# Kernel tuning notes

Measured on AMD Instinct MI355X. Metric: run time of the kernel, lower is better.

The kernel has to match this reference:

```python
import jax, jax.numpy as jnp
import numpy as np

T, B, DIM, N, K = 512, 32, 1024, 256, 32  # K = checkpoint interval, divides T


def setup_inputs() -> dict:
    key = jax.random.key(0)
    k1, k2, k3, k4 = jax.random.split(key, 4)
    scale = 1.0 / np.sqrt(DIM)  # keep projections O(1) like trained weights
    return {
        "x": jax.random.normal(k1, (T, B, DIM), dtype=jnp.float32),
        "S0": jnp.zeros((B, N, N), dtype=jnp.float32),
        "W_k": jax.random.normal(k2, (N, DIM), dtype=jnp.float32) * scale,
        "W_v": jax.random.normal(k3, (N, DIM), dtype=jnp.float32) * scale,
        "W_q": jax.random.normal(k4, (N, DIM), dtype=jnp.float32) * scale,
    }


def reference(x, S0, W_k, W_v, W_q):
    # Projections (batched GEMMs), done once up-front as in the torch code.
    k_all = jnp.einsum("tbd,nd->tbn", x, W_k)
    v_all = jnp.einsum("tbd,nd->tbn", x, W_v)
    q_all = jnp.einsum("tbd,nd->tbn", x, W_q)
    k_norm = k_all / (jnp.linalg.norm(k_all, axis=-1, keepdims=True) + 1e-6)

    def step(S, kvq):
        kn, v, q = kvq  # each [B, N]
        retrieved = jnp.einsum("bij,bj->bi", S, kn)          # S @ k_norm
        S = S + (v - retrieved)[:, :, None] * kn[:, None, :]  # rank-1 delta write
        Sq = jnp.einsum("bij,bj->bi", S, q)                   # readout with updated S
        out = Sq * jax.nn.silu(Sq)
        return S, out

    def segment(S, kvq_seg):
        return jax.lax.scan(step, S, kvq_seg)

    nseg = T // K
    seg_kvq = (
        k_norm.reshape(nseg, K, B, N),
        v_all.reshape(nseg, K, B, N),
        q_all.reshape(nseg, K, B, N),
    )
    _, outs = jax.lax.scan(segment, S0, seg_kvq)  # [nseg, K, B, N]
    return outs.reshape(T, B, N)
```

## Files before the change

kernel.cpp:

```cpp
#include <hip/hip_runtime.h>
#include <hip/hip_bf16.h>
#include <math.h>

#define T_DIM 512
#define B_DIM 32
#define D_DIM 1024
#define N_DIM 256
#define M_DIM (T_DIM * B_DIM)
#define CHUNK 32
#define NCHUNK (T_DIM / CHUNK)
#define IBLK 32
#define ST (B_DIM * N_DIM)
#define BK 32

typedef _Float16 f16;
typedef _Float16 f16x8 __attribute__((ext_vector_type(8)));
typedef _Float16 f16x4 __attribute__((ext_vector_type(4)));
typedef _Float16 f16x2 __attribute__((ext_vector_type(2)));
typedef __fp16   h16x2 __attribute__((ext_vector_type(2)));
typedef float    f32x4 __attribute__((ext_vector_type(4)));

#define LDK 264
#define LDT 40
#define LDV 36

#define GLOAD_LDS16(g, l)                                         \
  __builtin_amdgcn_global_load_lds(                               \
      (const __attribute__((address_space(1))) void*)(g),         \
      (__attribute__((address_space(3))) void*)(l), 16, 0, 0)

__device__ __forceinline__ f16x8 cvt8(const float4& a, const float4& b) {
  f16x8 h;
  h[0] = (f16)a.x; h[1] = (f16)a.y; h[2] = (f16)a.z; h[3] = (f16)a.w;
  h[4] = (f16)b.x; h[5] = (f16)b.y; h[6] = (f16)b.z; h[7] = (f16)b.w;
  return h;
}

__device__ __forceinline__ f16x8 pk8(const f32x4 a, const f32x4 b) {
  union { f16x8 v; h16x2 p[4]; } u;
  u.p[0] = __builtin_amdgcn_cvt_pkrtz(a[0], a[1]);
  u.p[1] = __builtin_amdgcn_cvt_pkrtz(a[2], a[3]);
  u.p[2] = __builtin_amdgcn_cvt_pkrtz(b[0], b[1]);
  u.p[3] = __builtin_amdgcn_cvt_pkrtz(b[2], b[3]);
  return u.v;
}

__global__ __launch_bounds__(256) void cvt_w_kernel(
    const float* __restrict__ wk, const float* __restrict__ wv,
    const float* __restrict__ wq, f16* __restrict__ out) {
  const int i = (blockIdx.x * 256 + threadIdx.x) * 8;
  const int m = blockIdx.y;
  const float* src = (m == 0) ? wk : (m == 1) ? wv : wq;
  const float4 f0 = *(const float4*)(src + i);
  const float4 f1 = *(const float4*)(src + i + 4);
  *(f16x8*)(out + (size_t)m * (N_DIM * D_DIM) + i) = cvt8(f0, f1);
}

__global__ __launch_bounds__(256, 3) void proj_gemm_mfma(
    const float* __restrict__ x, const f16* __restrict__ Wh,
    f16* __restrict__ ok, f16* __restrict__ ov, f16* __restrict__ oq) {
  __shared__ __align__(16) float Af[2][128 * BK];
  __shared__ __align__(16) f16   Bh[2][128 * BK];

  const int tid  = threadIdx.x;
  const int lane = tid & 63;
  const int w    = tid >> 6;
  const int wm   = w >> 1, wn = w & 1;
  const int lr   = lane & 15;
  const int lq   = lane >> 4;

  const int mb  = blockIdx.x * 128;
  const int mat = blockIdx.y >> 1;
  const int nb  = (blockIdx.y & 1) * 128;

  const f16* Wmat = Wh + (size_t)mat * (N_DIM * D_DIM) + (size_t)nb * D_DIM;
  f16*       C    = (mat == 0) ? ok : (mat == 1) ? ov : oq;

  const int ar  = lane >> 3;
  const int acq = (lane & 7) ^ ar;
  const int brr = lane >> 2;
  const int bco = lane & 3;

  f32x4 acc[4][4];
  #pragma unroll
  for (int i = 0; i < 4; ++i)
    #pragma unroll
    for (int j = 0; j < 4; ++j) acc[i][j] = (f32x4){0.f, 0.f, 0.f, 0.f};

  #pragma unroll
  for (int j = 0; j < 4; ++j) {
    const int r = 32 * j + 8 * w + ar;
    GLOAD_LDS16(x + (size_t)(mb + r) * D_DIM + acq * 4, &Af[0][(32 * j + 8 * w) * BK]);
  }
  #pragma unroll
  for (int j = 0; j < 2; ++j) {
    const int r = 64 * j + 16 * w + brr;
    GLOAD_LDS16(Wmat + (size_t)r * D_DIM + bco * 8, &Bh[0][(64 * j + 16 * w) * BK]);
  }
  __syncthreads();

  int cur = 0;
  for (int kt = 0; kt < D_DIM; kt += BK) {
    if (kt + BK < D_DIM) {
      #pragma unroll
      for (int j = 0; j < 4; ++j) {
        const int r = 32 * j + 8 * w + ar;
        GLOAD_LDS16(x + (size_t)(mb + r) * D_DIM + kt + BK + acq * 4,
                    &Af[cur ^ 1][(32 * j + 8 * w) * BK]);
      }
      #pragma unroll
      for (int j = 0; j < 2; ++j) {
        const int r = 64 * j + 16 * w + brr;
        GLOAD_LDS16(Wmat + (size_t)r * D_DIM + kt + BK + bco * 8,
                    &Bh[cur ^ 1][(64 * j + 16 * w) * BK]);
      }
    }
    {
      f16x8 af[4], bf[4];
      #pragma unroll
      for (int mi = 0; mi < 4; ++mi) {
        const int row = 64 * wm + 16 * mi + lr;
        const int q0  = (2 * lq)     ^ (row & 7);
        const int q1  = (2 * lq + 1) ^ (row & 7);
        const f32x4 a0 = *(const f32x4*)&Af[cur][row * BK + q0 * 4];
        const f32x4 a1 = *(const f32x4*)&Af[cur][row * BK + q1 * 4];
        af[mi] = pk8(a0, a1);
      }
      #pragma unroll
      for (int nj = 0; nj < 4; ++nj) {
        const int row = 64 * wn + 16 * nj + lr;
        bf[nj] = *(const f16x8*)&Bh[cur][row * BK + lq * 8];
      }
      #pragma unroll
      for (int mi = 0; mi < 4; ++mi)
        #pragma unroll
        for (int nj = 0; nj < 4; ++nj)
          acc[mi][nj] = __builtin_amdgcn_mfma_f32_16x16x32_f16(af[mi], bf[nj], acc[mi][nj], 0, 0, 0);
    }
    __syncthreads();
    cur ^= 1;
  }

  #pragma unroll
  for (int mi = 0; mi < 4; ++mi)
    #pragma unroll
    for (int nj = 0; nj < 4; ++nj)
      #pragma unroll
      for (int r = 0; r < 4; ++r) {
        const int rg = mb + 64 * wm + 16 * mi + 4 * lq + r;
        const int cg = nb + 64 * wn + 16 * nj + lr;
        C[(size_t)rg * N_DIM + cg] = (f16)acc[mi][nj][r];
      }
}

__global__ __launch_bounds__(256) void knorm_kernel(f16* __restrict__ k) {
  const int w    = threadIdx.x >> 6;
  const int lane = threadIdx.x & 63;
  const int row  = blockIdx.x * 4 + w;
  f16* p = k + (size_t)row * N_DIM + lane * 4;
  f16x4 h = *reinterpret_cast<const f16x4*>(p);
  const float x0 = (float)h[0], x1 = (float)h[1], x2 = (float)h[2], x3 = (float)h[3];
  float ss = x0 * x0 + x1 * x1 + x2 * x2 + x3 * x3;
  #pragma unroll
  for (int m = 1; m < 64; m <<= 1) ss += __shfl_xor(ss, m, 64);
  const float inv = 1.0f / (sqrtf(ss) + 1e-6f);
  h[0] = (f16)(x0 * inv); h[1] = (f16)(x1 * inv);
  h[2] = (f16)(x2 * inv); h[3] = (f16)(x3 * inv);
  *reinterpret_cast<f16x4*>(p) = h;
}

__global__ __launch_bounds__(256, 2) void precompute_wg(
    const f16* __restrict__ kn, const f16* __restrict__ q,
    f16* __restrict__ Wg, f16* __restrict__ Gg, f16* __restrict__ KTg) {
  __shared__ __align__(16) f16 Kh[32 * LDK];
  __shared__ __align__(16) f16 Qh[32 * LDK];
  __shared__ float Al[32 * 33];

  const int tid  = threadIdx.x;
  const int lane = tid & 63;
  const int w    = tid >> 6;
  const int lr   = lane & 15;
  const int lq   = lane >> 4;
  const int tm   = w >> 1, tn = w & 1;
  const int b    = blockIdx.x >> 4;
  const int c    = blockIdx.x & 15;
  const int t0g  = c * CHUNK;

  {
    const int t = tid >> 3, cg = tid & 7;
    const f16* ks = kn + (size_t)(t0g + t) * ST + b * N_DIM + cg * 32;
    const f16* qs = q  + (size_t)(t0g + t) * ST + b * N_DIM + cg * 32;
    #pragma unroll
    for (int m = 0; m < 4; ++m) {
      *(f16x8*)&Kh[t * LDK + cg * 32 + 8 * m] = ((const f16x8*)ks)[m];
      *(f16x8*)&Qh[t * LDK + cg * 32 + 8 * m] = ((const f16x8*)qs)[m];
    }
  }
  __syncthreads();

  {
    f16* kt_dst = KTg + ((size_t)blockIdx.x * N_DIM + tid) * CHUNK;
    #pragma unroll
    for (int t8 = 0; t8 < 4; ++t8) {
      f16x8 h;
      #pragma unroll
      for (int e = 0; e < 8; ++e) h[e] = Kh[(8 * t8 + e) * LDK + tid];
      *(f16x8*)(kt_dst + 8 * t8) = h;
    }
  }

  f32x4 Aa = {0.f, 0.f, 0.f, 0.f}, Ga = {0.f, 0.f, 0.f, 0.f};
  #pragma unroll
  for (int kk = 0; kk < 8; ++kk) {
    f16x8 ka = *(const f16x8*)&Kh[(16 * tm + lr) * LDK + 32 * kk + 8 * lq];
    f16x8 qa = *(const f16x8*)&Qh[(16 * tm + lr) * LDK + 32 * kk + 8 * lq];
    f16x8 kb = *(const f16x8*)&Kh[(16 * tn + lr) * LDK + 32 * kk + 8 * lq];
    Aa = __builtin_amdgcn_mfma_f32_16x16x32_f16(ka, kb, Aa, 0, 0, 0);
    Ga = __builtin_amdgcn_mfma_f32_16x16x32_f16(qa, kb, Ga, 0, 0, 0);
  }
  {
    const int s = 16 * tn + lr;
    f16* gdst = Gg + (size_t)blockIdx.x * 1280;
    #pragma unroll
    for (int r = 0; r < 4; ++r) {
      const int t = 16 * tm + 4 * lq + r;
      Al[t * 33 + s] = (s < t) ? Aa[r] : 0.f;
      gdst[t * LDT + s] = (f16)((s <= t) ? Ga[r] : 0.f);
    }
  }
  __syncthreads();

  if (tid < 32) {
    float wv[32];
    f16* wdst = Wg + (size_t)blockIdx.x * 1280;
    #pragma unroll
    for (int t = 0; t < 32; ++t) {
      float s0 = 0.f, s1 = 0.f, s2 = 0.f, s3 = 0.f;
      #pragma unroll
      for (int s = 0; s < 32; ++s) {
        if (s >= t) break;
        const float a = Al[t * 33 + s];
        if ((s & 3) == 0) s0 = fmaf(a, wv[s], s0);
        else if ((s & 3) == 1) s1 = fmaf(a, wv[s], s1);
        else if ((s & 3) == 2) s2 = fmaf(a, wv[s], s2);
        else s3 = fmaf(a, wv[s], s3);
      }
      wv[t] = ((t == tid) ? 1.f : 0.f) - ((s0 + s1) + (s2 + s3));
    }
    #pragma unroll
    for (int t = 0; t < 32; ++t) wdst[t * LDT + tid] = (f16)wv[t];
  }
}

__global__ __launch_bounds__(512, 1) void scan_chunked(
    const f16* __restrict__ kn, const f16* __restrict__ v,
    const f16* __restrict__ q, const float* __restrict__ S0,
    const f16* __restrict__ Wg, const f16* __restrict__ Gg,
    const f16* __restrict__ KTg, float* __restrict__ out) {
  __shared__ __align__(16) f16 Kh[32 * LDK];
  __shared__ __align__(16) f16 Qh[32 * LDK];
  __shared__ __align__(16) f16 Sh[32 * LDK];
  __shared__ __align__(16) f16 KhT[256 * LDT];
  __shared__ __align__(16) f16 Wl[32 * LDT];
  __shared__ __align__(16) f16 Gl[32 * LDT];
  __shared__ __align__(16) f16 U0T[32 * LDT];
  __shared__ __align__(16) f16 UT[32 * LDT];
  __shared__ __align__(16) float Vl[32 * LDV];

  const int tid  = threadIdx.x;
  const int lane = tid & 63;
  const int w    = tid >> 6;
  const int lr   = lane & 15;
  const int lq   = lane >> 4;
  const int role = w >> 2;
  const int w4   = w & 3;
  const int tm   = w4 >> 1, tn = w4 & 1;
  const int b    = blockIdx.x & 31;
  const int i0   = (blockIdx.x >> 5) * IBLK;

  f32x4 acc[2][2];
  const float* S0b = S0 + (size_t)b * N_DIM * N_DIM + (size_t)i0 * N_DIM;
  #pragma unroll
  for (int ti = 0; ti < 2; ++ti)
    #pragma unroll
    for (int jt = 0; jt < 2; ++jt)
      #pragma unroll
      for (int r = 0; r < 4; ++r) {
        const int i = 16 * ti + 4 * lq + r;
        const int j = 32 * w + 16 * jt + lr;
        acc[ti][jt][r] = S0b[(size_t)i * N_DIM + j];
      }
  {
    const int i = tid >> 4, cg = tid & 15;
    const float* ss = S0b + (size_t)i * N_DIM + cg * 16;
    #pragma unroll
    for (int m = 0; m < 2; ++m) {
      float4 f0 = *(const float4*)(ss + 8 * m);
      float4 f1 = *(const float4*)(ss + 8 * m + 4);
      *(f16x8*)&Sh[i * LDK + cg * 16 + 8 * m] = cvt8(f0, f1);
    }
  }
  __syncthreads();

  for (int c = 0; c < NCHUNK; ++c) {
    const int t0g = c * CHUNK;
    {
      const int t = tid >> 4, cg = tid & 15;
      const f16* ks = kn + (size_t)(t0g + t) * ST + b * N_DIM + cg * 16;
      const f16* qs = q  + (size_t)(t0g + t) * ST + b * N_DIM + cg * 16;
      #pragma unroll
      for (int m = 0; m < 2; ++m) {
        *(f16x8*)&Kh[t * LDK + cg * 16 + 8 * m] = ((const f16x8*)ks)[m];
        *(f16x8*)&Qh[t * LDK + cg * 16 + 8 * m] = ((const f16x8*)qs)[m];
      }
      const int c2 = (tid & 15) * 2;
      const f16x2 vf = *(const f16x2*)(v + (size_t)(t0g + t) * ST + b * N_DIM + i0 + c2);
      *(float2*)&Vl[t * LDV + c2] = make_float2((float)vf[0], (float)vf[1]);
    }
    {
      const int row = tid >> 1, m0 = (tid & 1) * 2;
      const f16* src = KTg + ((size_t)(b * NCHUNK + c) * N_DIM + row) * CHUNK;
      #pragma unroll
      for (int m = 0; m < 2; ++m)
        *(f16x8*)&KhT[row * LDT + 8 * (m0 + m)] = ((const f16x8*)src)[m0 + m];
    }
    if (tid < 160) {
      ((f16x8*)Wl)[tid] = ((const f16x8*)(Wg + (size_t)(b * NCHUNK + c) * 1280))[tid];
    } else if (tid < 320) {
      ((f16x8*)Gl)[tid - 160] = ((const f16x8*)(Gg + (size_t)(b * NCHUNK + c) * 1280))[tid - 160];
    }
    __syncthreads();

    f32x4 Oq = {0.f, 0.f, 0.f, 0.f};
    if (role == 0) {
      f32x4 Pacc = {0.f, 0.f, 0.f, 0.f};
      #pragma unroll
      for (int kk = 0; kk < 8; ++kk) {
        f16x8 ka = *(const f16x8*)&Kh[(16 * tm + lr) * LDK + 32 * kk + 8 * lq];
        f16x8 sb = *(const f16x8*)&Sh[(16 * tn + lr) * LDK + 32 * kk + 8 * lq];
        Pacc = __builtin_amdgcn_mfma_f32_16x16x32_f16(ka, sb, Pacc, 0, 0, 0);
      }
      const int i = 16 * tn + lr;
      const int t0 = 16 * tm + 4 * lq;
      f16x4 u0;
      #pragma unroll
      for (int r = 0; r < 4; ++r) u0[r] = (f16)(Vl[(t0 + r) * LDV + i] - Pacc[r]);
      *(f16x4*)&U0T[i * LDT + t0] = u0;
    } else {
      #pragma unroll
      for (int kk = 0; kk < 8; ++kk) {
        f16x8 qa = *(const f16x8*)&Qh[(16 * tm + lr) * LDK + 32 * kk + 8 * lq];
        f16x8 sb = *(const f16x8*)&Sh[(16 * tn + lr) * LDK + 32 * kk + 8 * lq];
        Oq = __builtin_amdgcn_mfma_f32_16x16x32_f16(qa, sb, Oq, 0, 0, 0);
      }
    }
    __syncthreads();

    if (role == 0) {
      f16x8 wa = *(const f16x8*)&Wl[(16 * tm + lr) * LDT + 8 * lq];
      f16x8 ub = *(const f16x8*)&U0T[(16 * tn + lr) * LDT + 8 * lq];
      f32x4 z = {0.f, 0.f, 0.f, 0.f};
      f32x4 Ud = __builtin_amdgcn_mfma_f32_16x16x32_f16(wa, ub, z, 0, 0, 0);
      const int i = 16 * tn + lr;
      const int t0 = 16 * tm + 4 * lq;
      f16x4 uh;
      #pragma unroll
      for (int r = 0; r < 4; ++r) uh[r] = (f16)Ud[r];
      *(f16x4*)&UT[i * LDT + t0] = uh;
    }
    __syncthreads();

    if (role == 1) {
      f16x8 ga = *(const f16x8*)&Gl[(16 * tm + lr) * LDT + 8 * lq];
      f16x8 ub = *(const f16x8*)&UT[(16 * tn + lr) * LDT + 8 * lq];
      f32x4 O = __builtin_amdgcn_mfma_f32_16x16x32_f16(ga, ub, Oq, 0, 0, 0);
      const int i = 16 * tn + lr;
      const int tt0 = 16 * tm + 4 * lq;
      #pragma unroll
      for (int r = 0; r < 4; ++r) {
        const float sq = O[r];
        const float sig = 1.0f / (1.0f + __expf(-sq));
        out[(size_t)(t0g + tt0 + r) * ST + b * N_DIM + i0 + i] = sq * sq * sig;
      }
    }
    #pragma unroll
    for (int ti = 0; ti < 2; ++ti) {
      f16x8 ua = *(const f16x8*)&UT[(16 * ti + lr) * LDT + 8 * lq];
      #pragma unroll
      for (int jt = 0; jt < 2; ++jt) {
        f16x8 kb = *(const f16x8*)&KhT[(32 * w + 16 * jt + lr) * LDT + 8 * lq];
        acc[ti][jt] = __builtin_amdgcn_mfma_f32_16x16x32_f16(ua, kb, acc[ti][jt], 0, 0, 0);
      }
    }
    #pragma unroll
    for (int ti = 0; ti < 2; ++ti)
      #pragma unroll
      for (int jt = 0; jt < 2; ++jt)
        #pragma unroll
        for (int r = 0; r < 4; ++r)
          Sh[(16 * ti + 4 * lq + r) * LDK + 32 * w + 16 * jt + lr] = (f16)acc[ti][jt][r];
    __syncthreads();
  }
}

extern "C" void kernel_launch(void* const* d_in, const int* in_sizes, int n_in,
                              void* d_out, int out_size, void* d_ws, size_t ws_size,
                              hipStream_t stream) {
  (void)in_sizes; (void)n_in; (void)out_size; (void)ws_size;
  const float* x  = (const float*)d_in[0];
  const float* S0 = (const float*)d_in[1];
  const float* Wk = (const float*)d_in[2];
  const float* Wv = (const float*)d_in[3];
  const float* Wq = (const float*)d_in[4];
  float* outp = (float*)d_out;

  f16* kn  = (f16*)d_ws;
  f16* vv  = kn + (size_t)M_DIM * N_DIM;
  f16* qq  = vv + (size_t)M_DIM * N_DIM;
  f16* Wg  = qq + (size_t)M_DIM * N_DIM;
  f16* Gg  = Wg + (size_t)B_DIM * NCHUNK * 1280;
  f16* KTg = Gg + (size_t)B_DIM * NCHUNK * 1280;
  f16* Wh  = KTg + (size_t)B_DIM * NCHUNK * N_DIM * CHUNK;

  dim3 gw(N_DIM * D_DIM / 8 / 256, 3);
  cvt_w_kernel<<<gw, 256, 0, stream>>>(Wk, Wv, Wq, Wh);
  dim3 gg(M_DIM / 128, 6);
  proj_gemm_mfma<<<gg, 256, 0, stream>>>(x, Wh, kn, vv, qq);
  knorm_kernel<<<M_DIM / 4, 256, 0, stream>>>(kn);
  precompute_wg<<<B_DIM * NCHUNK, 256, 0, stream>>>(kn, qq, Wg, Gg, KTg);
  scan_chunked<<<B_DIM * (N_DIM / IBLK), 512, 0, stream>>>(kn, vv, qq, S0, Wg, Gg, KTg, outp);
}
```

Measured before the change: 102.4 us.

## Triple-buffer projection GEMM LDS loads with a single barrier per k-step

Replaces the double-buffered LDS pipeline in the projection GEMM with a three-stage ring buffer. Each iteration waits with vmcnt(6), so only the oldest stage must land, then runs one barrier and issues the load two tiles ahead. This removes the second __syncthreads per iteration and keeps more global loads in flight. It raises LDS use and lowers the launch-bounds occupancy hint from 3 to 2 blocks per CU, which may reduce latency hiding across waves.

```diff
diff --git a/kernel.cpp b/kernel.cpp
--- a/kernel.cpp
+++ b/kernel.cpp
@@ -12,6 +12,7 @@
 #define IBLK 32
 #define ST (B_DIM * N_DIM)
 #define BK 32
+#define NT (D_DIM / BK)
 
 typedef _Float16 f16;
 typedef _Float16 f16x8 __attribute__((ext_vector_type(8)));
@@ -56,11 +57,11 @@
   *(f16x8*)(out + (size_t)m * (N_DIM * D_DIM) + i) = cvt8(f0, f1);
 }
 
-__global__ __launch_bounds__(256, 3) void proj_gemm_mfma(
+__global__ __launch_bounds__(256, 2) void proj_gemm_mfma(
     const float* __restrict__ x, const f16* __restrict__ Wh,
     f16* __restrict__ ok, f16* __restrict__ ov, f16* __restrict__ oq) {
-  __shared__ __align__(16) float Af[2][128 * BK];
-  __shared__ __align__(16) f16   Bh[2][128 * BK];
+  __shared__ __align__(16) float Af[3][128 * BK];
+  __shared__ __align__(16) f16   Bh[3][128 * BK];
 
   const int tid  = threadIdx.x;
   const int lane = tid & 63;
@@ -87,59 +88,71 @@
     #pragma unroll
     for (int j = 0; j < 4; ++j) acc[i][j] = (f32x4){0.f, 0.f, 0.f, 0.f};
 
-  #pragma unroll
-  for (int j = 0; j < 4; ++j) {
-    const int r = 32 * j + 8 * w + ar;
-    GLOAD_LDS16(x + (size_t)(mb + r) * D_DIM + acq * 4, &Af[0][(32 * j + 8 * w) * BK]);
-  }
-  #pragma unroll
-  for (int j = 0; j < 2; ++j) {
-    const int r = 64 * j + 16 * w + brr;
-    GLOAD_LDS16(Wmat + (size_t)r * D_DIM + bco * 8, &Bh[0][(64 * j + 16 * w) * BK]);
-  }
-  __syncthreads();
-
-  int cur = 0;
-  for (int kt = 0; kt < D_DIM; kt += BK) {
-    if (kt + BK < D_DIM) {
-      #pragma unroll
-      for (int j = 0; j < 4; ++j) {
-        const int r = 32 * j + 8 * w + ar;
-        GLOAD_LDS16(x + (size_t)(mb + r) * D_DIM + kt + BK + acq * 4,
-                    &Af[cur ^ 1][(32 * j + 8 * w) * BK]);
-      }
-      #pragma unroll
-      for (int j = 0; j < 2; ++j) {
-        const int r = 64 * j + 16 * w + brr;
-        GLOAD_LDS16(Wmat + (size_t)r * D_DIM + kt + BK + bco * 8,
-                    &Bh[cur ^ 1][(64 * j + 16 * w) * BK]);
-      }
-    }
-    {
-      f16x8 af[4], bf[4];
-      #pragma unroll
-      for (int mi = 0; mi < 4; ++mi) {
-        const int row = 64 * wm + 16 * mi + lr;
-        const int q0  = (2 * lq)     ^ (row & 7);
-        const int q1  = (2 * lq + 1) ^ (row & 7);
-        const f32x4 a0 = *(const f32x4*)&Af[cur][row * BK + q0 * 4];
-        const f32x4 a1 = *(const f32x4*)&Af[cur][row * BK + q1 * 4];
-        af[mi] = pk8(a0, a1);
-      }
-      #pragma unroll
-      for (int nj = 0; nj < 4; ++nj) {
-        const int row = 64 * wn + 16 * nj + lr;
-        bf[nj] = *(const f16x8*)&Bh[cur][row * BK + lq * 8];
-      }
-      #pragma unroll
-      for (int mi = 0; mi < 4; ++mi)
-        #pragma unroll
-        for (int nj = 0; nj < 4; ++nj)
-          acc[mi][nj] = __builtin_amdgcn_mfma_f32_16x16x32_f16(af[mi], bf[nj], acc[mi][nj], 0, 0, 0);
-    }
-    __syncthreads();
-    cur ^= 1;
-  }
+#define STAGE(t, bi)                                                         \
+  do {                                                                       \
+    const int kt_ = (t) * BK;                                                \
+    _Pragma("unroll")                                                        \
+    for (int j = 0; j < 4; ++j) {                                            \
+      const int r = 32 * j + 8 * w + ar;                                     \
+      GLOAD_LDS16(x + (size_t)(mb + r) * D_DIM + kt_ + acq * 4,              \
+                  &Af[bi][(32 * j + 8 * w) * BK]);                           \
+    }                                                                        \
+    _Pragma("unroll")                                                        \
+    for (int j = 0; j < 2; ++j) {                                            \
+      const int r = 64 * j + 16 * w + brr;                                   \
+      GLOAD_LDS16(Wmat + (size_t)r * D_DIM + kt_ + bco * 8,                  \
+                  &Bh[bi][(64 * j + 16 * w) * BK]);                          \
+    }                                                                        \
+  } while (0)
+
+#define COMPUTE(bi)                                                          \
+  do {                                                                       \
+    f16x8 af[4], bf[4];                                                      \
+    _Pragma("unroll")                                                        \
+    for (int mi = 0; mi < 4; ++mi) {                                         \
+      const int row = 64 * wm + 16 * mi + lr;                                \
+      const int q0  = (2 * lq)     ^ (row & 7);                              \
+      const int q1  = (2 * lq + 1) ^ (row & 7);                              \
+      const f32x4 a0 = *(const f32x4*)&Af[bi][row * BK + q0 * 4];            \
+      const f32x4 a1 = *(const f32x4*)&Af[bi][row * BK + q1 * 4];            \
+      af[mi] = pk8(a0, a1);                                                  \
+    }                                                                        \
+    _Pragma("unroll")                                                        \
+    for (int nj = 0; nj < 4; ++nj) {                                         \
+      const int row = 64 * wn + 16 * nj + lr;                                \
+      bf[nj] = *(const f16x8*)&Bh[bi][row * BK + lq * 8];                    \
+    }                                                                        \
+    _Pragma("unroll")                                                        \
+    for (int mi = 0; mi < 4; ++mi)                                           \
+      _Pragma("unroll")                                                      \
+      for (int nj = 0; nj < 4; ++nj)                                         \
+        acc[mi][nj] = __builtin_amdgcn_mfma_f32_16x16x32_f16(                \
+            af[mi], bf[nj], acc[mi][nj], 0, 0, 0);                           \
+  } while (0)
+
+  STAGE(0, 0);
+  STAGE(1, 1);
+
+  for (int k = 0; k < NT - 2; ++k) {
+    const int cb = k % 3;
+    const int nb3 = (k + 2) % 3;
+    asm volatile("s_waitcnt vmcnt(6)" ::: "memory");
+    __builtin_amdgcn_s_barrier();
+    __builtin_amdgcn_sched_barrier(0);
+    COMPUTE(cb);
+    STAGE(k + 2, nb3);
+  }
+  asm volatile("s_waitcnt vmcnt(6)" ::: "memory");
+  __builtin_amdgcn_s_barrier();
+  __builtin_amdgcn_sched_barrier(0);
+  COMPUTE((NT - 2) % 3);
+  asm volatile("s_waitcnt vmcnt(0)" ::: "memory");
+  __builtin_amdgcn_s_barrier();
+  __builtin_amdgcn_sched_barrier(0);
+  COMPUTE((NT - 1) % 3);
+
+#undef STAGE
+#undef COMPUTE
 
   #pragma unroll
   for (int mi = 0; mi < 4; ++mi)
```

After: 107.4 us. +4.8%, slower.

## Prefetch next chunk's operands into registers and drop the per-chunk load barrier

Applied to the files above, without the earlier changes.

The first chunk's K, Q, V, K-transpose, W and G tiles are now staged before the loop. Inside the loop, the next chunk's tiles are loaded from global memory into registers at the start of the current chunk's compute. Each register copy is written to shared memory right after the barrier that frees that buffer. This hides global-load latency behind the MFMA phases of the sequential recurrence and removes one __syncthreads per chunk, at the cost of extra live registers.

```diff
diff --git a/kernel.cpp b/kernel.cpp
--- a/kernel.cpp
+++ b/kernel.cpp
@@ -278,6 +278,10 @@
   const int b    = blockIdx.x & 31;
   const int i0   = (blockIdx.x >> 5) * IBLK;
 
+  const int st_t  = tid >> 4, st_cg = tid & 15;
+  const int st_c2 = (tid & 15) * 2;
+  const int kt_row = tid >> 1, kt_m0 = (tid & 1) * 2;
+
   f32x4 acc[2][2];
   const float* S0b = S0 + (size_t)b * N_DIM * N_DIM + (size_t)i0 * N_DIM;
   #pragma unroll
@@ -291,45 +295,54 @@
         acc[ti][jt][r] = S0b[(size_t)i * N_DIM + j];
       }
   {
-    const int i = tid >> 4, cg = tid & 15;
-    const float* ss = S0b + (size_t)i * N_DIM + cg * 16;
+    const float* ss = S0b + (size_t)st_t * N_DIM + st_cg * 16;
     #pragma unroll
     for (int m = 0; m < 2; ++m) {
       float4 f0 = *(const float4*)(ss + 8 * m);
       float4 f1 = *(const float4*)(ss + 8 * m + 4);
-      *(f16x8*)&Sh[i * LDK + cg * 16 + 8 * m] = cvt8(f0, f1);
+      *(f16x8*)&Sh[st_t * LDK + st_cg * 16 + 8 * m] = cvt8(f0, f1);
+    }
+  }
+  {
+    const f16* ks = kn + (size_t)st_t * ST + b * N_DIM + st_cg * 16;
+    const f16* qs = q  + (size_t)st_t * ST + b * N_DIM + st_cg * 16;
+    #pragma unroll
+    for (int m = 0; m < 2; ++m) {
+      *(f16x8*)&Kh[st_t * LDK + st_cg * 16 + 8 * m] = ((const f16x8*)ks)[m];
+      *(f16x8*)&Qh[st_t * LDK + st_cg * 16 + 8 * m] = ((const f16x8*)qs)[m];
+    }
+    const f16x2 vf = *(const f16x2*)(v + (size_t)st_t * ST + b * N_DIM + i0 + st_c2);
+    *(float2*)&Vl[st_t * LDV + st_c2] = make_float2((float)vf[0], (float)vf[1]);
+    const f16* src = KTg + ((size_t)(b * NCHUNK) * N_DIM + kt_row) * CHUNK;
+    #pragma unroll
+    for (int m = 0; m < 2; ++m)
+      *(f16x8*)&KhT[kt_row * LDT + 8 * (kt_m0 + m)] = ((const f16x8*)src)[kt_m0 + m];
+    if (tid < 160) {
+      ((f16x8*)Wl)[tid] = ((const f16x8*)(Wg + (size_t)(b * NCHUNK) * 1280))[tid];
+    } else if (tid < 320) {
+      ((f16x8*)Gl)[tid - 160] = ((const f16x8*)(Gg + (size_t)(b * NCHUNK) * 1280))[tid - 160];
     }
   }
   __syncthreads();
 
   for (int c = 0; c < NCHUNK; ++c) {
     const int t0g = c * CHUNK;
-    {
-      const int t = tid >> 4, cg = tid & 15;
-      const f16* ks = kn + (size_t)(t0g + t) * ST + b * N_DIM + cg * 16;
-      const f16* qs = q  + (size_t)(t0g + t) * ST + b * N_DIM + cg * 16;
-      #pragma unroll
-      for (int m = 0; m < 2; ++m) {
-        *(f16x8*)&Kh[t * LDK + cg * 16 + 8 * m] = ((const f16x8*)ks)[m];
-        *(f16x8*)&Qh[t * LDK + cg * 16 + 8 * m] = ((const f16x8*)qs)[m];
-      }
-      const int c2 = (tid & 15) * 2;
-      const f16x2 vf = *(const f16x2*)(v + (size_t)(t0g + t) * ST + b * N_DIM + i0 + c2);
-      *(float2*)&Vl[t * LDV + c2] = make_float2((float)vf[0], (float)vf[1]);
-    }
-    {
-      const int row = tid >> 1, m0 = (tid & 1) * 2;
-      const f16* src = KTg + ((size_t)(b * NCHUNK + c) * N_DIM + row) * CHUNK;
-      #pragma unroll
-      for (int m = 0; m < 2; ++m)
-        *(f16x8*)&KhT[row * LDT + 8 * (m0 + m)] = ((const f16x8*)src)[m0 + m];
-    }
-    if (tid < 160) {
-      ((f16x8*)Wl)[tid] = ((const f16x8*)(Wg + (size_t)(b * NCHUNK + c) * 1280))[tid];
-    } else if (tid < 320) {
-      ((f16x8*)Gl)[tid - 160] = ((const f16x8*)(Gg + (size_t)(b * NCHUNK + c) * 1280))[tid - 160];
-    }
-    __syncthreads();
+    const bool more = (c + 1) < NCHUNK;
+
+    f16x8 nk[2], nq[2], nkt[2], nwg;
+    f16x2 nv;
+    if (more) {
+      const f16* ks = kn + (size_t)(t0g + CHUNK + st_t) * ST + b * N_DIM + st_cg * 16;
+      const f16* qs = q  + (size_t)(t0g + CHUNK + st_t) * ST + b * N_DIM + st_cg * 16;
+      #pragma unroll
+      for (int m = 0; m < 2; ++m) { nk[m] = ((const f16x8*)ks)[m]; nq[m] = ((const f16x8*)qs)[m]; }
+      nv = *(const f16x2*)(v + (size_t)(t0g + CHUNK + st_t) * ST + b * N_DIM + i0 + st_c2);
+      const f16* src = KTg + ((size_t)(b * NCHUNK + c + 1) * N_DIM + kt_row) * CHUNK;
+      #pragma unroll
+      for (int m = 0; m < 2; ++m) nkt[m] = ((const f16x8*)src)[kt_m0 + m];
+      if (tid < 160)      nwg = ((const f16x8*)(Wg + (size_t)(b * NCHUNK + c + 1) * 1280))[tid];
+      else if (tid < 320) nwg = ((const f16x8*)(Gg + (size_t)(b * NCHUNK + c + 1) * 1280))[tid - 160];
+    }
 
     f32x4 Oq = {0.f, 0.f, 0.f, 0.f};
     if (role == 0) {
@@ -356,6 +369,14 @@
     }
     __syncthreads();
 
+    if (more) {
+      #pragma unroll
+      for (int m = 0; m < 2; ++m) {
+        *(f16x8*)&Kh[st_t * LDK + st_cg * 16 + 8 * m] = nk[m];
+        *(f16x8*)&Qh[st_t * LDK + st_cg * 16 + 8 * m] = nq[m];
+      }
+      *(float2*)&Vl[st_t * LDV + st_c2] = make_float2((float)nv[0], (float)nv[1]);
+    }
     if (role == 0) {
       f16x8 wa = *(const f16x8*)&Wl[(16 * tm + lr) * LDT + 8 * lq];
       f16x8 ub = *(const f16x8*)&U0T[(16 * tn + lr) * LDT + 8 * lq];
@@ -370,6 +391,8 @@
     }
     __syncthreads();
 
+    if (more && tid < 160) ((f16x8*)Wl)[tid] = nwg;
+
     if (role == 1) {
       f16x8 ga = *(const f16x8*)&Gl[(16 * tm + lr) * LDT + 8 * lq];
       f16x8 ub = *(const f16x8*)&UT[(16 * tn + lr) * LDT + 8 * lq];
@@ -400,6 +423,13 @@
         for (int r = 0; r < 4; ++r)
           Sh[(16 * ti + 4 * lq + r) * LDK + 32 * w + 16 * jt + lr] = (f16)acc[ti][jt][r];
     __syncthreads();
+
+    if (more) {
+      #pragma unroll
+      for (int m = 0; m < 2; ++m)
+        *(f16x8*)&KhT[kt_row * LDT + 8 * (kt_m0 + m)] = nkt[m];
+      if (tid >= 160 && tid < 320) ((f16x8*)Gl)[tid - 160] = nwg;
+    }
   }
 }
 
```

Result: faster. 92.32 us (median of 2 runs) (-9.9%).
